# Kernel tuning notes

Hardware: AMD Instinct MI355X
Metric: run time of the kernel (lower is better)

Reference implementation:

```python
import jax, jax.numpy as jnp
import numpy as np

N_NODES = 50000
N_EDGES = 200000
NODE_DIM = 32   # in_channels (== hidden_dim, required by NNConv nn output size)
EDGE_DIM = 16
HIDDEN = 32
OUT_DIM = 32
EPS = 1e-5
SLOPE = 0.01  # LeakyReLU default negative_slope


def setup_inputs() -> dict:
    key = jax.random.key(0)
    ks = jax.random.split(key, 16)
    inp = {
        "x": jax.random.normal(ks[0], (N_NODES, NODE_DIM), dtype=jnp.float32),
        "edge_index": jax.random.randint(ks[1], (2, N_EDGES), 0, N_NODES, dtype=jnp.int64),
        "edge_attr": jax.random.normal(ks[2], (N_EDGES, EDGE_DIM), dtype=jnp.float32),
        "batch": jnp.zeros((N_NODES,), dtype=jnp.int64),
        # edge MLP params
        "W1": jax.random.normal(ks[3], (EDGE_DIM, HIDDEN), dtype=jnp.float32) / np.sqrt(EDGE_DIM),
        "b1": jnp.zeros((HIDDEN,), dtype=jnp.float32),
        "bn1_gamma": jnp.ones((HIDDEN,), dtype=jnp.float32),
        "bn1_beta": jnp.zeros((HIDDEN,), dtype=jnp.float32),
        "bn1_mean": jax.random.normal(ks[4], (HIDDEN,), dtype=jnp.float32) * 0.1,
        "bn1_var": jax.random.uniform(ks[5], (HIDDEN,), dtype=jnp.float32, minval=0.5, maxval=1.5),
        "W2": jax.random.normal(ks[6], (HIDDEN, HIDDEN * OUT_DIM), dtype=jnp.float32) / np.sqrt(HIDDEN),
        "b2": jnp.zeros((HIDDEN * OUT_DIM,), dtype=jnp.float32),
        "bn2_gamma": jnp.ones((HIDDEN * OUT_DIM,), dtype=jnp.float32),
        "bn2_beta": jnp.zeros((HIDDEN * OUT_DIM,), dtype=jnp.float32),
        "bn2_mean": jax.random.normal(ks[7], (HIDDEN * OUT_DIM,), dtype=jnp.float32) * 0.1,
        "bn2_var": jax.random.uniform(ks[8], (HIDDEN * OUT_DIM,), dtype=jnp.float32, minval=0.5, maxval=1.5),
        # NNConv root weight + bias
        "root": jax.random.normal(ks[9], (NODE_DIM, OUT_DIM), dtype=jnp.float32) / np.sqrt(NODE_DIM),
        "bias": jnp.zeros((OUT_DIM,), dtype=jnp.float32),
    }
    return inp


def _leaky_relu(h):
    return jnp.where(h >= 0, h, SLOPE * h)


def _bn_eval(h, gamma, beta, mean, var):
    return (h - mean) * (gamma / jnp.sqrt(var + EPS)) + beta


def reference(x, edge_index, edge_attr, batch, W1, b1, bn1_gamma, bn1_beta, bn1_mean, bn1_var,
              W2, b2, bn2_gamma, bn2_beta, bn2_mean, bn2_var, root, bias):
    n_nodes = x.shape[0]
    # edge MLP (Dropout is identity in eval mode)
    h = edge_attr @ W1 + b1                                   # [E, H]
    h = _leaky_relu(_bn_eval(h, bn1_gamma, bn1_beta, bn1_mean, bn1_var))
    w = h @ W2 + b2                                           # [E, H*O]
    w = _leaky_relu(_bn_eval(w, bn2_gamma, bn2_beta, bn2_mean, bn2_var))
    w = w.reshape(-1, NODE_DIM, OUT_DIM)                      # [E, in, out]
    # gather source node features, per-edge bmm, scatter-add to destinations
    src, dst = edge_index[0], edge_index[1]
    x_j = x[src]                                              # [E, in]
    msg = jnp.einsum('ei,eio->eo', x_j, w)                    # [E, out]
    aggr = jax.ops.segment_sum(msg, dst, num_segments=n_nodes)
    return aggr + x @ root + bias
```

## Files before the change

kernel.cpp:

```cpp
#include <hip/hip_runtime.h>
#include <math.h>

#define ED 16
#define HD 32
#define OD 32
#define KD 1024
#define EPB 512
#define TPW 4
#define HPAD 34
#define CAP 32

typedef float  f32x4  __attribute__((ext_vector_type(4)));
typedef float  v4f    __attribute__((ext_vector_type(4)));
typedef short  bf16x8 __attribute__((ext_vector_type(8)));

constexpr size_t WS_WEIGHTS = 71808;
constexpr size_t OFF_MSG = 72064;

constexpr int LOFF_HX   = 0;
constexpr int LOFF_WHI  = EPB * HPAD * 2;
constexpr int LOFF_W1T  = LOFF_WHI + 32768;
constexpr int LOFF_B1   = LOFF_W1T + 2048;
constexpr int LOFF_BF   = LOFF_B1 + 128;
constexpr int LOFF_SRC  = LOFF_BF + 2048;
constexpr int LOFF_DST  = LOFF_SRC + 2048;
constexpr int LDS_TOTAL = LOFF_DST + 2048;

__device__ inline unsigned short bf16_rne(float v) {
    unsigned int u = __float_as_uint(v);
    return (unsigned short)((u + 0x7FFFu + ((u >> 16) & 1u)) >> 16);
}

__global__ __launch_bounds__(256)
void prep_root_kernel(const float* __restrict__ x, const float* __restrict__ root,
                      const float* __restrict__ bias, float* __restrict__ out, int nN,
                      int nRootBlk,
                      const float* __restrict__ W1, const float* __restrict__ b1,
                      const float* __restrict__ g1, const float* __restrict__ be1,
                      const float* __restrict__ m1, const float* __restrict__ v1,
                      const float* __restrict__ W2, const float* __restrict__ b2,
                      const float* __restrict__ g2, const float* __restrict__ be2,
                      const float* __restrict__ m2, const float* __restrict__ v2,
                      unsigned char* __restrict__ wsb)
{
    const int t = threadIdx.x;
    if ((int)blockIdx.x >= nRootBlk) {
        float* w1t = (float*)(wsb);
        float* b1f = (float*)(wsb + 2048);
        float* bf  = (float*)(wsb + 2176);
        unsigned short* ahi = (unsigned short*)(wsb + 6272);

        int bt = ((int)blockIdx.x - nRootBlk) * blockDim.x + t;
        int stride = 128 * blockDim.x;

        for (int q = bt; q < HD * ED; q += stride) {
            int c = q >> 4, j = q & 15;
            float s = g1[c] / sqrtf(v1[c] + 1e-5f);
            w1t[q] = W1[j * HD + c] * s;
        }
        for (int c = bt; c < HD; c += stride) {
            float s = g1[c] / sqrtf(v1[c] + 1e-5f);
            b1f[c] = b1[c] * s + be1[c] - m1[c] * s;
        }
        for (int k = bt; k < KD; k += stride) {
            float s = g2[k] / sqrtf(v2[k] + 1e-5f);
            bf[k] = b2[k] * s + be2[k] - m2[k] * s;
        }
        for (int p = bt; p < KD * HD; p += stride) {
            int j = p >> 10, k = p & 1023;
            float s = g2[k] / sqrtf(v2[k] + 1e-5f);
            float v = W2[p] * s;
            int g = k >> 4, m = k & 15;
            int quad = j >> 3, idx = j & 7;
            int q = g * 512 + (quad * 16 + m) * 8 + idx;
            ahi[q] = bf16_rne(v);
        }
        return;
    }

    __shared__ __align__(16) float rootS[HD * OD];
    __shared__ __align__(16) float biasS[OD];
    __shared__ float xsh[8][HD + 1];

    ((v4f*)rootS)[t] = ((const v4f*)root)[t];
    if (t < 8) ((v4f*)biasS)[t] = ((const v4f*)bias)[t];

    const int nodeBase = blockIdx.x * 8;
    if (t < 64) {
        int nl = t >> 3, q = t & 7;
        int node = nodeBase + nl;
        if (node >= nN) node = nN - 1;
        v4f v = ((const v4f*)(x + (size_t)node * HD))[q];
        xsh[nl][4 * q + 0] = v.x;
        xsh[nl][4 * q + 1] = v.y;
        xsh[nl][4 * q + 2] = v.z;
        xsh[nl][4 * q + 3] = v.w;
    }
    __syncthreads();

    const int nl = t >> 5, o = t & 31;
    const int node = nodeBase + nl;
    if (node >= nN) return;
    float acc = biasS[o];
#pragma unroll
    for (int i = 0; i < HD; ++i)
        acc = fmaf(xsh[nl][i], rootS[i * OD + o], acc);
    out[(size_t)node * OD + o] = acc;
}

template <bool MSG>
__global__ __launch_bounds__(512, 4)
void edge_kernel(const float* __restrict__ x, const int* __restrict__ eidx,
                 const float* __restrict__ ea_g, const unsigned char* __restrict__ wsb,
                 float* __restrict__ outm, int nE)
{
    __shared__ __align__(16) unsigned char smem[LDS_TOTAL];
    unsigned short* hHi = (unsigned short*)(smem + LOFF_HX);
    unsigned short* xS  = (unsigned short*)(smem + LOFF_HX);
    unsigned short* wLhi = (unsigned short*)(smem + LOFF_WHI);
    float* w1t = (float*)(smem + LOFF_W1T);
    float* b1s = (float*)(smem + LOFF_B1);
    float* bfL = (float*)(smem + LOFF_BF);
    int*  srcS = (int*)(smem + LOFF_SRC);
    int*  dstS = (int*)(smem + LOFF_DST);

    const int t = threadIdx.x;
    const int s = blockIdx.y;
    const float* wsW1 = (const float*)(wsb);
    const float* wsB1 = (const float*)(wsb + 2048);
    const float* wsBf = (const float*)(wsb + 2176);
    const unsigned short* wsAhi = (const unsigned short*)(wsb + 6272);

    int e = blockIdx.x * EPB + t;
    int ec = (e < nE) ? e : (nE - 1);
    int my_src = __builtin_nontemporal_load(eidx + ec);
    int my_dst = __builtin_nontemporal_load(eidx + nE + ec);

    const v4f* xrow_p = (const v4f*)(x + (size_t)my_src * HD);
    v4f xrow[8];
#pragma unroll
    for (int q = 0; q < 8; ++q) xrow[q] = xrow_p[q];

    const v4f* eap = (const v4f*)(ea_g + (size_t)ec * ED);
    v4f a0 = __builtin_nontemporal_load(eap + 0);
    v4f a1 = __builtin_nontemporal_load(eap + 1);
    v4f a2 = __builtin_nontemporal_load(eap + 2);
    v4f a3 = __builtin_nontemporal_load(eap + 3);

    srcS[t] = my_src;
    dstS[t] = my_dst;

    if (t < 128)       ((v4f*)w1t)[t] = ((const v4f*)wsW1)[t];
    else if (t < 136)  ((v4f*)b1s)[t - 128] = ((const v4f*)wsB1)[t - 128];
    else if (t < 264) {
        int d = t - 136;
        ((v4f*)bfL)[d] = ((const v4f*)wsBf)[(d >> 2) * 8 + s * 4 + (d & 3)];
    }

    {
        const v4f* srcHi = (const v4f*)wsAhi;
        v4f* dstHi = (v4f*)wLhi;
#pragma unroll
        for (int p = 0; p < 4; ++p) {
            int c = t + p * 512;
            int sc = (2 * (c >> 6) + s) * 64 + (c & 63);
            dstHi[c] = srcHi[sc];
        }
    }

    __syncthreads();

    float hreg[HD];
#pragma unroll
    for (int c = 0; c < HD; ++c) {
        const v4f* r4 = (const v4f*)(w1t + c * ED);
        v4f w0 = r4[0], w1 = r4[1], w2 = r4[2], w3 = r4[3];
        float acc = b1s[c];
        acc = fmaf(a0.x, w0.x, acc); acc = fmaf(a0.y, w0.y, acc);
        acc = fmaf(a0.z, w0.z, acc); acc = fmaf(a0.w, w0.w, acc);
        acc = fmaf(a1.x, w1.x, acc); acc = fmaf(a1.y, w1.y, acc);
        acc = fmaf(a1.z, w1.z, acc); acc = fmaf(a1.w, w1.w, acc);
        acc = fmaf(a2.x, w2.x, acc); acc = fmaf(a2.y, w2.y, acc);
        acc = fmaf(a2.z, w2.z, acc); acc = fmaf(a2.w, w2.w, acc);
        acc = fmaf(a3.x, w3.x, acc); acc = fmaf(a3.y, w3.y, acc);
        acc = fmaf(a3.z, w3.z, acc); acc = fmaf(a3.w, w3.w, acc);
        hreg[c] = fmaxf(acc, 0.01f * acc);
    }

#pragma unroll
    for (int ch = 0; ch < 4; ++ch) {
        bf16x8 phi;
#pragma unroll
        for (int u = 0; u < 8; ++u)
            phi[u] = (short)bf16_rne(hreg[ch * 8 + u]);
        *(bf16x8*)(hHi + t * HPAD + ch * 8) = phi;
    }
    __syncthreads();

    const int wave = t >> 6;
    const int lane = t & 63;
    const int n = lane & 15;
    const int quad = lane >> 4;
    const int ebase = wave * 64;

    bf16x8 bHi[TPW];
#pragma unroll
    for (int tt = 0; tt < TPW; ++tt) {
        int edge = ebase + tt * 16 + n;
        bHi[tt] = *(const bf16x8*)(hHi + edge * HPAD + quad * 8);
    }

    int xdst[TPW];
    bool evalid[TPW];
    int xoff[TPW];
    int geid[TPW];
#pragma unroll
    for (int tt = 0; tt < TPW; ++tt) {
        int le = ebase + tt * 16 + n;
        geid[tt] = blockIdx.x * EPB + le;
        evalid[tt] = geid[tt] < nE;
        xdst[tt] = dstS[le];
        xoff[tt] = le * HPAD;
    }

    __syncthreads();

#pragma unroll
    for (int ch = 0; ch < 4; ++ch) {
        bf16x8 px;
#pragma unroll
        for (int u = 0; u < 8; ++u) {
            int q = ch * 2 + (u >> 2);
            px[u] = (short)bf16_rne(xrow[q][u & 3]);
        }
        *(bf16x8*)(xS + t * HPAD + ch * 8) = px;
    }
    __syncthreads();

    f32x4 msg[TPW];
#pragma unroll
    for (int tt = 0; tt < TPW; ++tt)
        msg[tt] = (f32x4){0.f, 0.f, 0.f, 0.f};

#pragma unroll 4
    for (int i = 0; i < HD; ++i) {
        const bf16x8 cH = *(const bf16x8*)(wLhi + i * 512 + lane * 8);
        const f32x4 b0 = *(const f32x4*)(bfL + i * 16 + quad * 4);
        float xv[TPW];
#pragma unroll
        for (int tt = 0; tt < TPW; ++tt) {
            unsigned int u = xS[xoff[tt] + i];
            xv[tt] = __uint_as_float(u << 16);
        }

#pragma unroll
        for (int tt = 0; tt < TPW; ++tt) {
            f32x4 c = b0;
            c = __builtin_amdgcn_mfma_f32_16x16x32_bf16(cH, bHi[tt], c, 0, 0, 0);
            f32x4 w = __builtin_elementwise_max(c, 0.01f * c);
            f32x4 xs = {xv[tt], xv[tt], xv[tt], xv[tt]};
            msg[tt] = __builtin_elementwise_fma(xs, w, msg[tt]);
        }
    }

    if (MSG) {
#pragma unroll
        for (int tt = 0; tt < TPW; ++tt) {
            if (!evalid[tt]) continue;
            float* mp = outm + (size_t)geid[tt] * OD + s * 16 + quad * 4;
            __builtin_nontemporal_store(msg[tt], (f32x4*)mp);
        }
    } else {
#pragma unroll
        for (int tt = 0; tt < TPW; ++tt) {
            if (!evalid[tt]) continue;
            float* op = outm + (size_t)xdst[tt] * OD + s * 16 + quad * 4;
#pragma unroll
            for (int r = 0; r < 4; ++r)
                atomicAdd(op + r, msg[tt][r]);
        }
    }
}

__global__ void zero_cnt_kernel(int* __restrict__ cnt, int nN)
{
    int t = blockIdx.x * blockDim.x + threadIdx.x;
    if (t < nN) cnt[t] = 0;
}

__global__ void bucket_kernel(const int* __restrict__ eidx,
                              const float* __restrict__ msg,
                              float* __restrict__ out,
                              int* __restrict__ cnt, int* __restrict__ bucket, int nE)
{
    int e = blockIdx.x * blockDim.x + threadIdx.x;
    if (e >= nE) return;
    int dst = eidx[nE + e];
    int pos = atomicAdd(cnt + dst, 1);
    if (pos < CAP) {
        bucket[(size_t)dst * CAP + pos] = e;
    } else {
        const float* mp = msg + (size_t)e * OD;
        float* op = out + (size_t)dst * OD;
#pragma unroll
        for (int ch = 0; ch < OD; ++ch) atomicAdd(op + ch, mp[ch]);
    }
}

__global__ __launch_bounds__(256)
void gather_kernel(const float* __restrict__ msg, const int* __restrict__ bucket,
                   const int* __restrict__ cnt, float* __restrict__ out, int nN)
{
    int t = threadIdx.x;
    int v = blockIdx.x * 8 + (t >> 5);
    int ch = t & 31;
    if (v >= nN) return;
    int c = cnt[v];
    if (c > CAP) c = CAP;
    const int* bk = bucket + (size_t)v * CAP;
    float acc = 0.f;
    for (int p = 0; p < c; ++p) {
        int e = bk[p];
        acc += msg[(size_t)e * OD + ch];
    }
    out[(size_t)v * OD + ch] += acc;
}

__global__ __launch_bounds__(64)
void edge_kernel_raw(const float* __restrict__ x, const int* __restrict__ eidx,
                     const float* __restrict__ ea_g,
                     const float* __restrict__ W1, const float* __restrict__ b1,
                     const float* __restrict__ g1, const float* __restrict__ be1,
                     const float* __restrict__ m1, const float* __restrict__ v1,
                     const float* __restrict__ W2, const float* __restrict__ b2,
                     const float* __restrict__ g2, const float* __restrict__ be2,
                     const float* __restrict__ m2, const float* __restrict__ v2,
                     float* __restrict__ out, int nE)
{
    int e = blockIdx.x * 64 + threadIdx.x;
    if (e >= nE) return;
    const int obase = blockIdx.y * 16;

    int src = eidx[e];
    int dst = eidx[nE + e];

    float ea[ED];
#pragma unroll
    for (int j = 0; j < ED; ++j) ea[j] = ea_g[(size_t)e * ED + j];

    float h[HD];
#pragma unroll
    for (int c = 0; c < HD; ++c) {
        float acc = b1[c];
#pragma unroll
        for (int j = 0; j < ED; ++j) acc = fmaf(ea[j], W1[j * HD + c], acc);
        float s = g1[c] / sqrtf(v1[c] + 1e-5f);
        acc = (acc - m1[c]) * s + be1[c];
        h[c] = fmaxf(acc, 0.01f * acc);
    }

    float msg[16];
#pragma unroll
    for (int o = 0; o < 16; ++o) msg[o] = 0.f;

    const float* xj = x + (size_t)src * HD;
    for (int i = 0; i < HD; ++i) {
        float xv = xj[i];
#pragma unroll
        for (int oo = 0; oo < 16; ++oo) {
            int k = i * OD + obase + oo;
            float acc = b2[k];
#pragma unroll
            for (int j = 0; j < HD; ++j) acc = fmaf(h[j], W2[j * KD + k], acc);
            float s = g2[k] / sqrtf(v2[k] + 1e-5f);
            acc = (acc - m2[k]) * s + be2[k];
            float w = fmaxf(acc, 0.01f * acc);
            msg[oo] = fmaf(xv, w, msg[oo]);
        }
    }

    float* op = out + (size_t)dst * OD + obase;
#pragma unroll
    for (int oo = 0; oo < 16; ++oo) atomicAdd(op + oo, msg[oo]);
}

extern "C" void kernel_launch(void* const* d_in, const int* in_sizes, int n_in,
                              void* d_out, int out_size, void* d_ws, size_t ws_size,
                              hipStream_t stream)
{
    const float* x    = (const float*)d_in[0];
    const int*   eidx = (const int*)  d_in[1];
    const float* ea   = (const float*)d_in[2];
    const float* W1   = (const float*)d_in[4];
    const float* b1   = (const float*)d_in[5];
    const float* g1   = (const float*)d_in[6];
    const float* be1  = (const float*)d_in[7];
    const float* m1   = (const float*)d_in[8];
    const float* v1   = (const float*)d_in[9];
    const float* W2   = (const float*)d_in[10];
    const float* b2   = (const float*)d_in[11];
    const float* g2   = (const float*)d_in[12];
    const float* be2  = (const float*)d_in[13];
    const float* m2   = (const float*)d_in[14];
    const float* v2   = (const float*)d_in[15];
    const float* root = (const float*)d_in[16];
    const float* bias = (const float*)d_in[17];
    float* out = (float*)d_out;

    int nN = in_sizes[0] / HD;
    int nE = in_sizes[2] / ED;

    size_t msgB = (size_t)nE * OD * 4;
    size_t bktB = (size_t)nN * CAP * 4;
    size_t OFF_BKT = OFF_MSG + msgB;
    size_t OFF_CNT = OFF_BKT + bktB;
    size_t needTwoPhase = OFF_CNT + (size_t)nN * 4;

    if (ws_size >= needTwoPhase) {
        unsigned char* wsb = (unsigned char*)d_ws;
        float* msg  = (float*)(wsb + OFF_MSG);
        int* bucket = (int*)(wsb + OFF_BKT);
        int* cnt    = (int*)(wsb + OFF_CNT);

        int nRootBlk = (nN + 7) / 8;
        prep_root_kernel<<<dim3(nRootBlk + 128), 256, 0, stream>>>(
            x, root, bias, out, nN, nRootBlk,
            W1, b1, g1, be1, m1, v1, W2, b2, g2, be2, m2, v2, wsb);
        zero_cnt_kernel<<<(nN + 1023) / 1024, 1024, 0, stream>>>(cnt, nN);
        int nblk = (nE + EPB - 1) / EPB;
        edge_kernel<true><<<dim3(nblk, 2), 512, 0, stream>>>(x, eidx, ea, wsb, msg, nE);
        bucket_kernel<<<(nE + 255) / 256, 256, 0, stream>>>(eidx, msg, out, cnt, bucket, nE);
        gather_kernel<<<(nN + 7) / 8, 256, 0, stream>>>(msg, bucket, cnt, out, nN);
    } else if (ws_size >= WS_WEIGHTS) {
        unsigned char* wsb = (unsigned char*)d_ws;
        int nRootBlk = (nN + 7) / 8;
        prep_root_kernel<<<dim3(nRootBlk + 128), 256, 0, stream>>>(
            x, root, bias, out, nN, nRootBlk,
            W1, b1, g1, be1, m1, v1, W2, b2, g2, be2, m2, v2, wsb);
        int nblk = (nE + EPB - 1) / EPB;
        edge_kernel<false><<<dim3(nblk, 2), 512, 0, stream>>>(x, eidx, ea, wsb, out, nE);
    } else {
        prep_root_kernel<<<dim3((nN + 7) / 8), 256, 0, stream>>>(
            x, root, bias, out, nN, (nN + 7) / 8 + 1,
            W1, b1, g1, be1, m1, v1, W2, b2, g2, be2, m2, v2, (unsigned char*)d_ws);
        edge_kernel_raw<<<dim3((nE + 63) / 64, 2), 64, 0, stream>>>(
            x, eidx, ea, W1, b1, g1, be1, m1, v1,
            W2, b2, g2, be2, m2, v2, out, nE);
    }
}
```

Before: 203.9 us.

## Fuse bucketing into edge kernel, store bf16 messages, merge root into gather

Restructures the two-phase path. Per-destination bucket insertion now happens inside the edge kernel, and per-edge messages are stored as bf16 instead of fp32. The root transform and bias are folded into the gather kernel, and count zeroing is folded into a weight-prep kernel. This removes the separate zero, bucket and root launches and halves message traffic, at the cost of extra bf16 rounding in the messages. Overflowed nodes fall back to a slow scan over all edges.

```diff
diff --git a/kernel.cpp b/kernel.cpp
--- a/kernel.cpp
+++ b/kernel.cpp
@@ -13,6 +13,7 @@
 typedef float  f32x4  __attribute__((ext_vector_type(4)));
 typedef float  v4f    __attribute__((ext_vector_type(4)));
 typedef short  bf16x8 __attribute__((ext_vector_type(8)));
+typedef short  bf16x4 __attribute__((ext_vector_type(4)));
 
 constexpr size_t WS_WEIGHTS = 71808;
 constexpr size_t OFF_MSG = 72064;
@@ -29,6 +30,293 @@
 __device__ inline unsigned short bf16_rne(float v) {
     unsigned int u = __float_as_uint(v);
     return (unsigned short)((u + 0x7FFFu + ((u >> 16) & 1u)) >> 16);
+}
+
+__global__ __launch_bounds__(256)
+void prep_kernel(const float* __restrict__ W1, const float* __restrict__ b1,
+                 const float* __restrict__ g1, const float* __restrict__ be1,
+                 const float* __restrict__ m1, const float* __restrict__ v1,
+                 const float* __restrict__ W2, const float* __restrict__ b2,
+                 const float* __restrict__ g2, const float* __restrict__ be2,
+                 const float* __restrict__ m2, const float* __restrict__ v2,
+                 unsigned char* __restrict__ wsb, int* __restrict__ cnt, int nN)
+{
+    float* w1t = (float*)(wsb);
+    float* b1f = (float*)(wsb + 2048);
+    float* bf  = (float*)(wsb + 2176);
+    unsigned short* ahi = (unsigned short*)(wsb + 6272);
+
+    int bt = blockIdx.x * blockDim.x + threadIdx.x;
+    int stride = gridDim.x * blockDim.x;
+
+    for (int q = bt; q < nN; q += stride) cnt[q] = 0;
+
+    for (int q = bt; q < HD * ED; q += stride) {
+        int c = q >> 4, j = q & 15;
+        float s = g1[c] / sqrtf(v1[c] + 1e-5f);
+        w1t[q] = W1[j * HD + c] * s;
+    }
+    for (int c = bt; c < HD; c += stride) {
+        float s = g1[c] / sqrtf(v1[c] + 1e-5f);
+        b1f[c] = b1[c] * s + be1[c] - m1[c] * s;
+    }
+    for (int k = bt; k < KD; k += stride) {
+        float s = g2[k] / sqrtf(v2[k] + 1e-5f);
+        bf[k] = b2[k] * s + be2[k] - m2[k] * s;
+    }
+    for (int p = bt; p < KD * HD; p += stride) {
+        int j = p >> 10, k = p & 1023;
+        float s = g2[k] / sqrtf(v2[k] + 1e-5f);
+        float v = W2[p] * s;
+        int g = k >> 4, m = k & 15;
+        int quad = j >> 3, idx = j & 7;
+        int q = g * 512 + (quad * 16 + m) * 8 + idx;
+        ahi[q] = bf16_rne(v);
+    }
+}
+
+template <bool MSG>
+__global__ __launch_bounds__(512, 4)
+void edge_kernel(const float* __restrict__ x, const int* __restrict__ eidx,
+                 const float* __restrict__ ea_g, const unsigned char* __restrict__ wsb,
+                 float* __restrict__ out_atomic, unsigned short* __restrict__ msgb,
+                 int* __restrict__ cnt, int* __restrict__ bucket, int nE)
+{
+    __shared__ __align__(16) unsigned char smem[LDS_TOTAL];
+    unsigned short* hHi = (unsigned short*)(smem + LOFF_HX);
+    unsigned short* xS  = (unsigned short*)(smem + LOFF_HX);
+    unsigned short* wLhi = (unsigned short*)(smem + LOFF_WHI);
+    float* w1t = (float*)(smem + LOFF_W1T);
+    float* b1s = (float*)(smem + LOFF_B1);
+    float* bfL = (float*)(smem + LOFF_BF);
+    int*  srcS = (int*)(smem + LOFF_SRC);
+    int*  dstS = (int*)(smem + LOFF_DST);
+
+    const int t = threadIdx.x;
+    const int s = blockIdx.y;
+    const float* wsW1 = (const float*)(wsb);
+    const float* wsB1 = (const float*)(wsb + 2048);
+    const float* wsBf = (const float*)(wsb + 2176);
+    const unsigned short* wsAhi = (const unsigned short*)(wsb + 6272);
+
+    int e = blockIdx.x * EPB + t;
+    int ec = (e < nE) ? e : (nE - 1);
+    int my_src = __builtin_nontemporal_load(eidx + ec);
+    int my_dst = __builtin_nontemporal_load(eidx + nE + ec);
+
+    const v4f* xrow_p = (const v4f*)(x + (size_t)my_src * HD);
+    v4f xrow[8];
+#pragma unroll
+    for (int q = 0; q < 8; ++q) xrow[q] = xrow_p[q];
+
+    const v4f* eap = (const v4f*)(ea_g + (size_t)ec * ED);
+    v4f a0 = __builtin_nontemporal_load(eap + 0);
+    v4f a1 = __builtin_nontemporal_load(eap + 1);
+    v4f a2 = __builtin_nontemporal_load(eap + 2);
+    v4f a3 = __builtin_nontemporal_load(eap + 3);
+
+    srcS[t] = my_src;
+    dstS[t] = my_dst;
+
+    if (t < 128)       ((v4f*)w1t)[t] = ((const v4f*)wsW1)[t];
+    else if (t < 136)  ((v4f*)b1s)[t - 128] = ((const v4f*)wsB1)[t - 128];
+    else if (t < 264) {
+        int d = t - 136;
+        ((v4f*)bfL)[d] = ((const v4f*)wsBf)[(d >> 2) * 8 + s * 4 + (d & 3)];
+    }
+
+    {
+        const v4f* srcHi = (const v4f*)wsAhi;
+        v4f* dstHi = (v4f*)wLhi;
+#pragma unroll
+        for (int p = 0; p < 4; ++p) {
+            int c = t + p * 512;
+            int sc = (2 * (c >> 6) + s) * 64 + (c & 63);
+            dstHi[c] = srcHi[sc];
+        }
+    }
+
+    __syncthreads();
+
+    float hreg[HD];
+#pragma unroll
+    for (int c = 0; c < HD; ++c) {
+        const v4f* r4 = (const v4f*)(w1t + c * ED);
+        v4f w0 = r4[0], w1 = r4[1], w2 = r4[2], w3 = r4[3];
+        float acc = b1s[c];
+        acc = fmaf(a0.x, w0.x, acc); acc = fmaf(a0.y, w0.y, acc);
+        acc = fmaf(a0.z, w0.z, acc); acc = fmaf(a0.w, w0.w, acc);
+        acc = fmaf(a1.x, w1.x, acc); acc = fmaf(a1.y, w1.y, acc);
+        acc = fmaf(a1.z, w1.z, acc); acc = fmaf(a1.w, w1.w, acc);
+        acc = fmaf(a2.x, w2.x, acc); acc = fmaf(a2.y, w2.y, acc);
+        acc = fmaf(a2.z, w2.z, acc); acc = fmaf(a2.w, w2.w, acc);
+        acc = fmaf(a3.x, w3.x, acc); acc = fmaf(a3.y, w3.y, acc);
+        acc = fmaf(a3.z, w3.z, acc); acc = fmaf(a3.w, w3.w, acc);
+        hreg[c] = fmaxf(acc, 0.01f * acc);
+    }
+
+#pragma unroll
+    for (int ch = 0; ch < 4; ++ch) {
+        bf16x8 phi;
+#pragma unroll
+        for (int u = 0; u < 8; ++u)
+            phi[u] = (short)bf16_rne(hreg[ch * 8 + u]);
+        *(bf16x8*)(hHi + t * HPAD + ch * 8) = phi;
+    }
+    __syncthreads();
+
+    const int wave = t >> 6;
+    const int lane = t & 63;
+    const int n = lane & 15;
+    const int quad = lane >> 4;
+    const int ebase = wave * 64;
+
+    bf16x8 bHi[TPW];
+#pragma unroll
+    for (int tt = 0; tt < TPW; ++tt) {
+        int edge = ebase + tt * 16 + n;
+        bHi[tt] = *(const bf16x8*)(hHi + edge * HPAD + quad * 8);
+    }
+
+    int xdst[TPW];
+    bool evalid[TPW];
+    int xoff[TPW];
+    int geid[TPW];
+#pragma unroll
+    for (int tt = 0; tt < TPW; ++tt) {
+        int le = ebase + tt * 16 + n;
+        geid[tt] = blockIdx.x * EPB + le;
+        evalid[tt] = geid[tt] < nE;
+        xdst[tt] = dstS[le];
+        xoff[tt] = le * HPAD;
+    }
+
+    __syncthreads();
+
+#pragma unroll
+    for (int ch = 0; ch < 4; ++ch) {
+        bf16x8 px;
+#pragma unroll
+        for (int u = 0; u < 8; ++u) {
+            int q = ch * 2 + (u >> 2);
+            px[u] = (short)bf16_rne(xrow[q][u & 3]);
+        }
+        *(bf16x8*)(xS + t * HPAD + ch * 8) = px;
+    }
+    __syncthreads();
+
+    f32x4 msg[TPW];
+#pragma unroll
+    for (int tt = 0; tt < TPW; ++tt)
+        msg[tt] = (f32x4){0.f, 0.f, 0.f, 0.f};
+
+#pragma unroll 4
+    for (int i = 0; i < HD; ++i) {
+        const bf16x8 cH = *(const bf16x8*)(wLhi + i * 512 + lane * 8);
+        const f32x4 b0 = *(const f32x4*)(bfL + i * 16 + quad * 4);
+        float xv[TPW];
+#pragma unroll
+        for (int tt = 0; tt < TPW; ++tt) {
+            unsigned int u = xS[xoff[tt] + i];
+            xv[tt] = __uint_as_float(u << 16);
+        }
+
+#pragma unroll
+        for (int tt = 0; tt < TPW; ++tt) {
+            f32x4 c = b0;
+            c = __builtin_amdgcn_mfma_f32_16x16x32_bf16(cH, bHi[tt], c, 0, 0, 0);
+            f32x4 w = __builtin_elementwise_max(c, 0.01f * c);
+            f32x4 xs = {xv[tt], xv[tt], xv[tt], xv[tt]};
+            msg[tt] = __builtin_elementwise_fma(xs, w, msg[tt]);
+        }
+    }
+
+    if (MSG) {
+#pragma unroll
+        for (int tt = 0; tt < TPW; ++tt) {
+            if (!evalid[tt]) continue;
+            bf16x4 pm;
+#pragma unroll
+            for (int r = 0; r < 4; ++r) pm[r] = (short)bf16_rne(msg[tt][r]);
+            __builtin_nontemporal_store(pm,
+                (bf16x4*)(msgb + (size_t)geid[tt] * OD + s * 16 + quad * 4));
+        }
+        if (s == 0 && quad == 0) {
+#pragma unroll
+            for (int tt = 0; tt < TPW; ++tt) {
+                if (!evalid[tt]) continue;
+                int pos = atomicAdd(cnt + xdst[tt], 1);
+                if (pos < CAP) bucket[(size_t)xdst[tt] * CAP + pos] = geid[tt];
+            }
+        }
+    } else {
+#pragma unroll
+        for (int tt = 0; tt < TPW; ++tt) {
+            if (!evalid[tt]) continue;
+            float* op = out_atomic + (size_t)xdst[tt] * OD + s * 16 + quad * 4;
+#pragma unroll
+            for (int r = 0; r < 4; ++r)
+                atomicAdd(op + r, msg[tt][r]);
+        }
+    }
+}
+
+__global__ __launch_bounds__(256)
+void gather_root_kernel(const float* __restrict__ x, const float* __restrict__ root,
+                        const float* __restrict__ bias,
+                        const unsigned short* __restrict__ msgb,
+                        const int* __restrict__ bucket, const int* __restrict__ cnt,
+                        const int* __restrict__ eidx,
+                        float* __restrict__ out, int nN, int nE)
+{
+    __shared__ __align__(16) float rootS[HD * OD];
+    __shared__ __align__(16) float biasS[OD];
+    __shared__ float xsh[8][HD + 1];
+
+    const int t = threadIdx.x;
+    ((v4f*)rootS)[t] = ((const v4f*)root)[t];
+    if (t < 8) ((v4f*)biasS)[t] = ((const v4f*)bias)[t];
+
+    const int nodeBase = blockIdx.x * 8;
+    if (t < 64) {
+        int nl = t >> 3, q = t & 7;
+        int node = nodeBase + nl;
+        if (node >= nN) node = nN - 1;
+        v4f v = ((const v4f*)(x + (size_t)node * HD))[q];
+        xsh[nl][4 * q + 0] = v.x;
+        xsh[nl][4 * q + 1] = v.y;
+        xsh[nl][4 * q + 2] = v.z;
+        xsh[nl][4 * q + 3] = v.w;
+    }
+    __syncthreads();
+
+    const int nl = t >> 5, ch = t & 31;
+    const int v = nodeBase + nl;
+    if (v >= nN) return;
+
+    float acc = biasS[ch];
+#pragma unroll
+    for (int i = 0; i < HD; ++i)
+        acc = fmaf(xsh[nl][i], rootS[i * OD + ch], acc);
+
+    int c = cnt[v];
+    if (c <= CAP) {
+        const int* bk = bucket + (size_t)v * CAP;
+        for (int p = 0; p < c; ++p) {
+            int e = bk[p];
+            unsigned int u = msgb[(size_t)e * OD + ch];
+            acc += __uint_as_float(u << 16);
+        }
+    } else {
+        const int* dstp = eidx + nE;
+        for (int e = 0; e < nE; ++e) {
+            if (dstp[e] == v) {
+                unsigned int u = msgb[(size_t)e * OD + ch];
+                acc += __uint_as_float(u << 16);
+            }
+        }
+    }
+    __builtin_nontemporal_store(acc, out + (size_t)v * OD + ch);
 }
 
 __global__ __launch_bounds__(256)
@@ -106,224 +394,6 @@
     for (int i = 0; i < HD; ++i)
         acc = fmaf(xsh[nl][i], rootS[i * OD + o], acc);
     out[(size_t)node * OD + o] = acc;
-}
-
-template <bool MSG>
-__global__ __launch_bounds__(512, 4)
-void edge_kernel(const float* __restrict__ x, const int* __restrict__ eidx,
-                 const float* __restrict__ ea_g, const unsigned char* __restrict__ wsb,
-                 float* __restrict__ outm, int nE)
-{
-    __shared__ __align__(16) unsigned char smem[LDS_TOTAL];
-    unsigned short* hHi = (unsigned short*)(smem + LOFF_HX);
-    unsigned short* xS  = (unsigned short*)(smem + LOFF_HX);
-    unsigned short* wLhi = (unsigned short*)(smem + LOFF_WHI);
-    float* w1t = (float*)(smem + LOFF_W1T);
-    float* b1s = (float*)(smem + LOFF_B1);
-    float* bfL = (float*)(smem + LOFF_BF);
-    int*  srcS = (int*)(smem + LOFF_SRC);
-    int*  dstS = (int*)(smem + LOFF_DST);
-
-    const int t = threadIdx.x;
-    const int s = blockIdx.y;
-    const float* wsW1 = (const float*)(wsb);
-    const float* wsB1 = (const float*)(wsb + 2048);
-    const float* wsBf = (const float*)(wsb + 2176);
-    const unsigned short* wsAhi = (const unsigned short*)(wsb + 6272);
-
-    int e = blockIdx.x * EPB + t;
-    int ec = (e < nE) ? e : (nE - 1);
-    int my_src = __builtin_nontemporal_load(eidx + ec);
-    int my_dst = __builtin_nontemporal_load(eidx + nE + ec);
-
-    const v4f* xrow_p = (const v4f*)(x + (size_t)my_src * HD);
-    v4f xrow[8];
-#pragma unroll
-    for (int q = 0; q < 8; ++q) xrow[q] = xrow_p[q];
-
-    const v4f* eap = (const v4f*)(ea_g + (size_t)ec * ED);
-    v4f a0 = __builtin_nontemporal_load(eap + 0);
-    v4f a1 = __builtin_nontemporal_load(eap + 1);
-    v4f a2 = __builtin_nontemporal_load(eap + 2);
-    v4f a3 = __builtin_nontemporal_load(eap + 3);
-
-    srcS[t] = my_src;
-    dstS[t] = my_dst;
-
-    if (t < 128)       ((v4f*)w1t)[t] = ((const v4f*)wsW1)[t];
-    else if (t < 136)  ((v4f*)b1s)[t - 128] = ((const v4f*)wsB1)[t - 128];
-    else if (t < 264) {
-        int d = t - 136;
-        ((v4f*)bfL)[d] = ((const v4f*)wsBf)[(d >> 2) * 8 + s * 4 + (d & 3)];
-    }
-
-    {
-        const v4f* srcHi = (const v4f*)wsAhi;
-        v4f* dstHi = (v4f*)wLhi;
-#pragma unroll
-        for (int p = 0; p < 4; ++p) {
-            int c = t + p * 512;
-            int sc = (2 * (c >> 6) + s) * 64 + (c & 63);
-            dstHi[c] = srcHi[sc];
-        }
-    }
-
-    __syncthreads();
-
-    float hreg[HD];
-#pragma unroll
-    for (int c = 0; c < HD; ++c) {
-        const v4f* r4 = (const v4f*)(w1t + c * ED);
-        v4f w0 = r4[0], w1 = r4[1], w2 = r4[2], w3 = r4[3];
-        float acc = b1s[c];
-        acc = fmaf(a0.x, w0.x, acc); acc = fmaf(a0.y, w0.y, acc);
-        acc = fmaf(a0.z, w0.z, acc); acc = fmaf(a0.w, w0.w, acc);
-        acc = fmaf(a1.x, w1.x, acc); acc = fmaf(a1.y, w1.y, acc);
-        acc = fmaf(a1.z, w1.z, acc); acc = fmaf(a1.w, w1.w, acc);
-        acc = fmaf(a2.x, w2.x, acc); acc = fmaf(a2.y, w2.y, acc);
-        acc = fmaf(a2.z, w2.z, acc); acc = fmaf(a2.w, w2.w, acc);
-        acc = fmaf(a3.x, w3.x, acc); acc = fmaf(a3.y, w3.y, acc);
-        acc = fmaf(a3.z, w3.z, acc); acc = fmaf(a3.w, w3.w, acc);
-        hreg[c] = fmaxf(acc, 0.01f * acc);
-    }
-
-#pragma unroll
-    for (int ch = 0; ch < 4; ++ch) {
-        bf16x8 phi;
-#pragma unroll
-        for (int u = 0; u < 8; ++u)
-            phi[u] = (short)bf16_rne(hreg[ch * 8 + u]);
-        *(bf16x8*)(hHi + t * HPAD + ch * 8) = phi;
-    }
-    __syncthreads();
-
-    const int wave = t >> 6;
-    const int lane = t & 63;
-    const int n = lane & 15;
-    const int quad = lane >> 4;
-    const int ebase = wave * 64;
-
-    bf16x8 bHi[TPW];
-#pragma unroll
-    for (int tt = 0; tt < TPW; ++tt) {
-        int edge = ebase + tt * 16 + n;
-        bHi[tt] = *(const bf16x8*)(hHi + edge * HPAD + quad * 8);
-    }
-
-    int xdst[TPW];
-    bool evalid[TPW];
-    int xoff[TPW];
-    int geid[TPW];
-#pragma unroll
-    for (int tt = 0; tt < TPW; ++tt) {
-        int le = ebase + tt * 16 + n;
-        geid[tt] = blockIdx.x * EPB + le;
-        evalid[tt] = geid[tt] < nE;
-        xdst[tt] = dstS[le];
-        xoff[tt] = le * HPAD;
-    }
-
-    __syncthreads();
-
-#pragma unroll
-    for (int ch = 0; ch < 4; ++ch) {
-        bf16x8 px;
-#pragma unroll
-        for (int u = 0; u < 8; ++u) {
-            int q = ch * 2 + (u >> 2);
-            px[u] = (short)bf16_rne(xrow[q][u & 3]);
-        }
-        *(bf16x8*)(xS + t * HPAD + ch * 8) = px;
-    }
-    __syncthreads();
-
-    f32x4 msg[TPW];
-#pragma unroll
-    for (int tt = 0; tt < TPW; ++tt)
-        msg[tt] = (f32x4){0.f, 0.f, 0.f, 0.f};
-
-#pragma unroll 4
-    for (int i = 0; i < HD; ++i) {
-        const bf16x8 cH = *(const bf16x8*)(wLhi + i * 512 + lane * 8);
-        const f32x4 b0 = *(const f32x4*)(bfL + i * 16 + quad * 4);
-        float xv[TPW];
-#pragma unroll
-        for (int tt = 0; tt < TPW; ++tt) {
-            unsigned int u = xS[xoff[tt] + i];
-            xv[tt] = __uint_as_float(u << 16);
-        }
-
-#pragma unroll
-        for (int tt = 0; tt < TPW; ++tt) {
-            f32x4 c = b0;
-            c = __builtin_amdgcn_mfma_f32_16x16x32_bf16(cH, bHi[tt], c, 0, 0, 0);
-            f32x4 w = __builtin_elementwise_max(c, 0.01f * c);
-            f32x4 xs = {xv[tt], xv[tt], xv[tt], xv[tt]};
-            msg[tt] = __builtin_elementwise_fma(xs, w, msg[tt]);
-        }
-    }
-
-    if (MSG) {
-#pragma unroll
-        for (int tt = 0; tt < TPW; ++tt) {
-            if (!evalid[tt]) continue;
-            float* mp = outm + (size_t)geid[tt] * OD + s * 16 + quad * 4;
-            __builtin_nontemporal_store(msg[tt], (f32x4*)mp);
-        }
-    } else {
-#pragma unroll
-        for (int tt = 0; tt < TPW; ++tt) {
-            if (!evalid[tt]) continue;
-            float* op = outm + (size_t)xdst[tt] * OD + s * 16 + quad * 4;
-#pragma unroll
-            for (int r = 0; r < 4; ++r)
-                atomicAdd(op + r, msg[tt][r]);
-        }
-    }
-}
-
-__global__ void zero_cnt_kernel(int* __restrict__ cnt, int nN)
-{
-    int t = blockIdx.x * blockDim.x + threadIdx.x;
-    if (t < nN) cnt[t] = 0;
-}
-
-__global__ void bucket_kernel(const int* __restrict__ eidx,
-                              const float* __restrict__ msg,
-                              float* __restrict__ out,
-                              int* __restrict__ cnt, int* __restrict__ bucket, int nE)
-{
-    int e = blockIdx.x * blockDim.x + threadIdx.x;
-    if (e >= nE) return;
-    int dst = eidx[nE + e];
-    int pos = atomicAdd(cnt + dst, 1);
-    if (pos < CAP) {
-        bucket[(size_t)dst * CAP + pos] = e;
-    } else {
-        const float* mp = msg + (size_t)e * OD;
-        float* op = out + (size_t)dst * OD;
-#pragma unroll
-        for (int ch = 0; ch < OD; ++ch) atomicAdd(op + ch, mp[ch]);
-    }
-}
-
-__global__ __launch_bounds__(256)
-void gather_kernel(const float* __restrict__ msg, const int* __restrict__ bucket,
-                   const int* __restrict__ cnt, float* __restrict__ out, int nN)
-{
-    int t = threadIdx.x;
-    int v = blockIdx.x * 8 + (t >> 5);
-    int ch = t & 31;
-    if (v >= nN) return;
-    int c = cnt[v];
-    if (c > CAP) c = CAP;
-    const int* bk = bucket + (size_t)v * CAP;
-    float acc = 0.f;
-    for (int p = 0; p < c; ++p) {
-        int e = bk[p];
-        acc += msg[(size_t)e * OD + ch];
-    }
-    out[(size_t)v * OD + ch] += acc;
 }
 
 __global__ __launch_bounds__(64)
@@ -410,27 +480,25 @@
     int nN = in_sizes[0] / HD;
     int nE = in_sizes[2] / ED;
 
-    size_t msgB = (size_t)nE * OD * 4;
+    size_t msgB = (size_t)nE * OD * 2;
     size_t bktB = (size_t)nN * CAP * 4;
-    size_t OFF_BKT = OFF_MSG + msgB;
+    size_t OFF_BKT = (OFF_MSG + msgB + 15) & ~(size_t)15;
     size_t OFF_CNT = OFF_BKT + bktB;
     size_t needTwoPhase = OFF_CNT + (size_t)nN * 4;
 
     if (ws_size >= needTwoPhase) {
         unsigned char* wsb = (unsigned char*)d_ws;
-        float* msg  = (float*)(wsb + OFF_MSG);
+        unsigned short* msgb = (unsigned short*)(wsb + OFF_MSG);
         int* bucket = (int*)(wsb + OFF_BKT);
         int* cnt    = (int*)(wsb + OFF_CNT);
 
-        int nRootBlk = (nN + 7) / 8;
-        prep_root_kernel<<<dim3(nRootBlk + 128), 256, 0, stream>>>(
-            x, root, bias, out, nN, nRootBlk,
-            W1, b1, g1, be1, m1, v1, W2, b2, g2, be2, m2, v2, wsb);
-        zero_cnt_kernel<<<(nN + 1023) / 1024, 1024, 0, stream>>>(cnt, nN);
+        prep_kernel<<<128, 256, 0, stream>>>(
+            W1, b1, g1, be1, m1, v1, W2, b2, g2, be2, m2, v2, wsb, cnt, nN);
         int nblk = (nE + EPB - 1) / EPB;
-        edge_kernel<true><<<dim3(nblk, 2), 512, 0, stream>>>(x, eidx, ea, wsb, msg, nE);
-        bucket_kernel<<<(nE + 255) / 256, 256, 0, stream>>>(eidx, msg, out, cnt, bucket, nE);
-        gather_kernel<<<(nN + 7) / 8, 256, 0, stream>>>(msg, bucket, cnt, out, nN);
+        edge_kernel<true><<<dim3(nblk, 2), 512, 0, stream>>>(
+            x, eidx, ea, wsb, nullptr, msgb, cnt, bucket, nE);
+        gather_root_kernel<<<(nN + 7) / 8, 256, 0, stream>>>(
+            x, root, bias, msgb, bucket, cnt, eidx, out, nN, nE);
     } else if (ws_size >= WS_WEIGHTS) {
         unsigned char* wsb = (unsigned char*)d_ws;
         int nRootBlk = (nN + 7) / 8;
@@ -438,7 +506,8 @@
             x, root, bias, out, nN, nRootBlk,
             W1, b1, g1, be1, m1, v1, W2, b2, g2, be2, m2, v2, wsb);
         int nblk = (nE + EPB - 1) / EPB;
-        edge_kernel<false><<<dim3(nblk, 2), 512, 0, stream>>>(x, eidx, ea, wsb, out, nE);
+        edge_kernel<false><<<dim3(nblk, 2), 512, 0, stream>>>(
+            x, eidx, ea, wsb, out, nullptr, nullptr, nullptr, nE);
     } else {
         prep_root_kernel<<<dim3((nN + 7) / 8), 256, 0, stream>>>(
             x, root, bias, out, nN, (nN + 7) / 8 + 1,
```

After: 184.3 us. 9.6% less time.
